# Optimization experiments

Hardware: AMD Instinct MI355X
Metric: run time of the kernel (lower is better)

## Reference

```python
import jax, jax.numpy as jnp
import numpy as np

SIGMA = 16.0


def setup_inputs() -> dict:
    key = jax.random.key(0)
    k1, k2, k3 = jax.random.split(key, 3)
    B, T, D = 8, 2048, 1024
    x = jax.random.normal(k1, (B, T, D), dtype=jnp.float32)
    posv = jax.random.randint(k2, (B, T), 0, 64, dtype=jnp.int32)
    posh = jax.random.randint(k3, (B, T), 0, 64, dtype=jnp.int32)
    return {"x": x, "posv": posv, "posh": posh}


def reference(x, posv, posh):
    # pos: [B, T, 2] float, as in torch.stack([posv, posh], -1).float()
    pos = jnp.stack([posv, posh], axis=-1).astype(jnp.float32)
    # pairwise squared distances: [B, T, T]
    diff = pos[:, :, None, :] - pos[:, None, :, :]
    dist_sq = jnp.sum(diff * diff, axis=-1)
    kernel = jnp.exp(-dist_sq / (2.0 * SIGMA * SIGMA))
    kernel = kernel / jnp.sum(kernel, axis=-1, keepdims=True)
    # dropout is identity in eval mode
    return jnp.einsum("bts,bsd->btd", kernel, x)
```

## Files before the change

kernel.cpp:

```cpp
#include <hip/hip_runtime.h>
#include <hip/hip_bf16.h>

#define NB 8
#define NT 2048
#define ND 1024
#define CAP 2048

typedef unsigned short ushort_t;
using short8 = __attribute__((ext_vector_type(8))) short;
using f32x4  = __attribute__((ext_vector_type(4))) float;

__device__ __forceinline__ ushort_t f2bf(float f) {
    __hip_bfloat16 h = __float2bfloat16(f);
    return *reinterpret_cast<ushort_t*>(&h);
}
__device__ __forceinline__ float bf2f(ushort_t u) {
    unsigned int v = ((unsigned int)u) << 16;
    return __int_as_float((int)v);
}


#define OFF_G2     256
#define OFF_AFH    768
#define OFF_AFL    8960
#define OFF_CNTV   17152
#define OFF_CNTH   19200
#define OFF_INVDEN 21248
#define OFF_GOFF   152320
#define OFF_TOKV   160512
#define OFF_TOKH   4354816
#define OFF_TOKV2  8549120
#define OFF_B1     12743424
#define B1_SLAB    ((size_t)64 * 64 * 1024 * 2)

__global__ __launch_bounds__(256) void k1_bucket(
    const int* __restrict__ posv, const int* __restrict__ posh,
    int* __restrict__ tokv, int* __restrict__ tokh,
    int* __restrict__ cntv, int* __restrict__ cnth,
    float* __restrict__ gbase, ushort_t* __restrict__ AfH,
    ushort_t* __restrict__ AfL)
{
    int b    = blockIdx.x >> 5;
    int blk  = blockIdx.x & 31;
    int wave = threadIdx.x >> 6;
    int lane = threadIdx.x & 63;

    if (blockIdx.x == 0) {
        if (threadIdx.x < 192) {
            int k = (int)threadIdx.x - 64;
            float v = 0.0f;
            if (k >= 0 && k < 127) {
                int r = k - 63;
                v = expf(-(float)(r * r) * (1.0f / 512.0f));
            }
            gbase[threadIdx.x] = v;
        }
#pragma unroll
        for (int p = 0; p < 16; p++) {
            int pos = (p << 8) + (int)threadIdx.x;
            int i   = pos & 7;
            int ln  = (pos >> 3) & 63;
            int ks  = (pos >> 9) & 1;
            int w   = pos >> 10;
            int q   = (w << 4) + (ln & 15);
            int k   = (ks << 5) + ((i >> 2) << 4) + ((ln >> 4) << 2) + (i & 3);
            int dlt = q - k;
            float g = expf(-(float)(dlt * dlt) * (1.0f / 512.0f));
            ushort_t hi = f2bf(g);
            AfH[pos] = hi;
            AfL[pos] = f2bf(g - bf2f(hi));
        }
    }

    int task   = blk * 4 + wave;
    int bucket = task & 63;
    int use_ph = task >> 6;
    const int* pos  = use_ph ? posh : posv;
    const int* opos = use_ph ? posv : posh;
    int* tok = (use_ph ? tokh : tokv) + ((size_t)(b * 64 + bucket)) * CAP;
    int* cnt = use_ph ? cnth : cntv;

    int vals[32];
#pragma unroll
    for (int k = 0; k < 32; k++) vals[k] = pos[b * NT + k * 64 + lane];

    unsigned long long lmask = (1ull << lane) - 1ull;
    int cursor = 0;
#pragma unroll 4
    for (int k = 0; k < 32; k++) {
        bool hit = (vals[k] == bucket);
        unsigned long long m = __ballot(hit);
        if (hit) {
            int t = k * 64 + lane;
            tok[cursor + __popcll(m & lmask)] = t | (opos[b * NT + t] << 16);
        }
        cursor += (int)__popcll(m);
    }
    if (lane == 0) cnt[b * 64 + bucket] = cursor;
}

__global__ __launch_bounds__(256) void k1b_group(
    const int* __restrict__ tokv, const int* __restrict__ cntv,
    int* __restrict__ tokv2, int4* __restrict__ goff)
{
    int bucket = blockIdx.x * 4 + (threadIdx.x >> 6);
    int lane   = threadIdx.x & 63;
    int n = cntv[bucket];
    const int* src = tokv + (size_t)bucket * CAP;
    int* dst = tokv2 + (size_t)bucket * CAP;
    unsigned long long lmask = (1ull << lane) - 1ull;

    int cnt0 = 0, cnt1 = 0, cnt2 = 0, cnt3 = 0;
    for (int base = 0; base < n; base += 64) {
        bool valid = base + lane < n;
        int pk = valid ? src[base + lane] : 0;
        int grp = (pk >> 20) & 3;
        cnt0 += (int)__popcll(__ballot(valid && grp == 0));
        cnt1 += (int)__popcll(__ballot(valid && grp == 1));
        cnt2 += (int)__popcll(__ballot(valid && grp == 2));
        cnt3 += (int)__popcll(__ballot(valid && grp == 3));
    }
    int s1 = cnt0, s2 = cnt0 + cnt1, s3 = cnt0 + cnt1 + cnt2;
    if (lane == 0) goff[bucket] = make_int4(0, s1, s2, s3);

    int c0 = 0, c1 = s1, c2 = s2, c3 = s3;
    for (int base = 0; base < n; base += 64) {
        bool valid = base + lane < n;
        int pk = valid ? src[base + lane] : 0;
        int grp = (pk >> 20) & 3;
        unsigned long long m0 = __ballot(valid && grp == 0);
        unsigned long long m1 = __ballot(valid && grp == 1);
        unsigned long long m2 = __ballot(valid && grp == 2);
        unsigned long long m3 = __ballot(valid && grp == 3);
        if (valid) {
            int p;
            if      (grp == 0) p = c0 + (int)__popcll(m0 & lmask);
            else if (grp == 1) p = c1 + (int)__popcll(m1 & lmask);
            else if (grp == 2) p = c2 + (int)__popcll(m2 & lmask);
            else               p = c3 + (int)__popcll(m3 & lmask);
            dst[p] = pk;
        }
        c0 += (int)__popcll(m0); c1 += (int)__popcll(m1);
        c2 += (int)__popcll(m2); c3 += (int)__popcll(m3);
    }
}

__global__ __launch_bounds__(256) void kden(
    const int* __restrict__ posv, const int* __restrict__ posh,
    const float* __restrict__ G2f, float* __restrict__ invden, int b0)
{
    int b   = b0 + (blockIdx.x >> 3);
    int phg = blockIdx.x & 7;
    int tid = threadIdx.x;

    __shared__ int   hist[64][64];
    __shared__ float g2s[128];
    __shared__ float tmp[64][8];

#pragma unroll
    for (int k = 0; k < 16; k++) ((int*)hist)[tid + (k << 8)] = 0;
    if (tid < 128) g2s[tid] = G2f[tid];
    __syncthreads();
#pragma unroll
    for (int k = 0; k < 8; k++) {
        int t = (k << 8) + tid;
        atomicAdd(&hist[posv[b * NT + t]][posh[b * NT + t]], 1);
    }
    __syncthreads();
#pragma unroll
    for (int c = 0; c < 2; c++) {
        int cell = (c << 8) + tid;
        int j    = cell >> 3;
        int phl  = cell & 7;
        int ph   = (phg << 3) + phl;
        float s = 0.f;
        for (int k = 0; k < 64; k++)
            s += (float)hist[j][k] * g2s[63 + k - ph];
        tmp[j][phl] = s;
    }
    __syncthreads();
#pragma unroll
    for (int c = 0; c < 2; c++) {
        int cell = (c << 8) + tid;
        int pv   = cell >> 3;
        int phl  = cell & 7;
        int ph   = (phg << 3) + phl;
        float s = 0.f;
        for (int j = 0; j < 64; j++)
            s += g2s[63 + j - pv] * tmp[j][phl];
        invden[(b * 64 + pv) * 64 + ph] = 1.0f / s;
    }
}

__device__ __forceinline__ short8 ldsBfrag(const ushort_t* rowp, int ks, int g4) {
    const ushort_t* p = rowp + (ks << 5) + g4;
    uint2 lo = *(const uint2*)(p);
    uint2 hi = *(const uint2*)(p + 16);
    uint4 pk; pk.x = lo.x; pk.y = lo.y; pk.z = hi.x; pk.w = hi.y;
    return __builtin_bit_cast(short8, pk);
}

__global__ __launch_bounds__(256) void k2_convh(
    const float* __restrict__ x,
    const int* __restrict__ tokv2, const int* __restrict__ cntv,
    const int4* __restrict__ goff,
    const ushort_t* __restrict__ AfH, const ushort_t* __restrict__ AfL,
    ushort_t* __restrict__ B1, int b0)
{
    int pv   = blockIdx.x & 63;
    int dc   = (blockIdx.x >> 6) & 15;
    int b    = b0 + (blockIdx.x >> 10);
    int tid  = threadIdx.x;
    int lane = tid & 63;
    int w    = tid >> 6;
    int d0   = dc << 6;

    __shared__ float    S[64][65];
    __shared__ ushort_t S16[64][68];

#pragma unroll
    for (int k = 0; k < 17; k++) {
        int idx = (k << 8) + tid;
        if (idx < 64 * 65) ((float*)S)[idx] = 0.f;
    }
    __syncthreads();

    int bucket = (b << 6) + pv;
    int n = cntv[bucket];
    const int* toks = tokv2 + (size_t)bucket * CAP;
    const float* xb = x + (((size_t)b * NT) << 10) + d0 + lane;

    int4 go = goff[bucket];
    int gs = (w == 0) ? go.x : (w == 1) ? go.y : (w == 2) ? go.z : go.w;
    int ge = (w == 3) ? n   : (w == 0) ? go.y : (w == 1) ? go.z : go.w;

    for (int win = gs; win < ge; win += 64) {
        int wn  = ge - win; if (wn > 64) wn = 64;
        int pkv = toks[win + lane];
        for (int i = 0; i < wn; i += 8) {
            int m = wn - i; if (m > 8) m = 8;
            int pk[8]; float xv[8];
#pragma unroll
            for (int j = 0; j < 8; j++)
                pk[j] = __builtin_amdgcn_readlane(pkv, i + j);
#pragma unroll
            for (int j = 0; j < 8; j++)
                if (j < m) xv[j] = xb[(size_t)(pk[j] & 0xffff) << 10];
#pragma unroll
            for (int j = 0; j < 8; j++)
                if (j < m) S[lane][pk[j] >> 16] += xv[j];
        }
    }
    __syncthreads();

    {
        int r  = tid & 63;
        int c0 = (tid >> 6) << 4;
#pragma unroll
        for (int c = 0; c < 16; c++)
            S16[r][c0 + c] = f2bf(S[r][c0 + c]);
    }
    __syncthreads();

    short8 ahi[2], alo[2];
#pragma unroll
    for (int ks = 0; ks < 2; ks++) {
        int idx = ((((w << 1) + ks) << 6) + lane) << 3;
        ahi[ks] = *(const short8*)(AfH + idx);
        alo[ks] = *(const short8*)(AfL + idx);
    }
    int g4 = (lane >> 4) << 2;
    int qbase = (w << 4) + g4;

    f32x4 accs[4];
#pragma unroll
    for (int nt = 0; nt < 4; nt++) {
        const ushort_t* rowp = &S16[(nt << 4) + (lane & 15)][0];
        f32x4 acc = {0.f, 0.f, 0.f, 0.f};
#pragma unroll
        for (int ks = 0; ks < 2; ks++) {
            short8 bf = ldsBfrag(rowp, ks, g4);
            acc = __builtin_amdgcn_mfma_f32_16x16x32_bf16(ahi[ks], bf, acc, 0, 0, 0);
            acc = __builtin_amdgcn_mfma_f32_16x16x32_bf16(alo[ks], bf, acc, 0, 0, 0);
        }
        accs[nt] = acc;
    }
    __syncthreads();

#pragma unroll
    for (int nt = 0; nt < 4; nt++)
#pragma unroll
        for (int reg = 0; reg < 4; reg++)
            S16[qbase + reg][(nt << 4) + (lane & 15)] = f2bf(accs[nt][reg]);
    __syncthreads();

    ushort_t* B1p = B1 + (((size_t)(b - b0)) << 22) + (((size_t)pv) << 10) + d0;
#pragma unroll
    for (int pass = 0; pass < 2; pass++) {
        int row = (pass << 5) + (tid >> 3);
        int col = (tid & 7) << 3;
        uint4 v = *(const uint4*)(&S16[row][col]);
        *reinterpret_cast<uint4*>(B1p + ((size_t)row << 16) + col) = v;
    }
}

__global__ __launch_bounds__(256) void k3_convv(
    const int* __restrict__ tokh, const int* __restrict__ cnth,
    const ushort_t* __restrict__ AfH, const ushort_t* __restrict__ AfL,
    const ushort_t* __restrict__ B1, const float* __restrict__ invden,
    float* __restrict__ out, int b0)
{
    int ph   = blockIdx.x & 63;
    int dc   = (blockIdx.x >> 6) & 15;
    int b    = b0 + (blockIdx.x >> 10);
    int tid  = threadIdx.x;
    int lane = tid & 63;
    int w    = tid >> 6;
    int d0   = dc << 6;

    int n = cnth[(b << 6) + ph];
    if (n == 0) return;

    __shared__ ushort_t u16[64][68];
    __shared__ float    y[64][65];

    const ushort_t* B1b = B1 + (((size_t)(b - b0)) << 22) + (((size_t)ph) << 16)
                        + d0 + lane;
#pragma unroll
    for (int it = 0; it < 16; it++) {
        int j = (w << 4) + it;
        u16[lane][j] = B1b[(size_t)j << 10];
    }
    __syncthreads();

    short8 ahi[2], alo[2];
#pragma unroll
    for (int ks = 0; ks < 2; ks++) {
        int idx = ((((w << 1) + ks) << 6) + lane) << 3;
        ahi[ks] = *(const short8*)(AfH + idx);
        alo[ks] = *(const short8*)(AfL + idx);
    }
    int g4 = (lane >> 4) << 2;
    int qbase = (w << 4) + g4;

#pragma unroll
    for (int nt = 0; nt < 4; nt++) {
        const ushort_t* rowp = &u16[(nt << 4) + (lane & 15)][0];
        f32x4 acc = {0.f, 0.f, 0.f, 0.f};
#pragma unroll
        for (int ks = 0; ks < 2; ks++) {
            short8 bf = ldsBfrag(rowp, ks, g4);
            acc = __builtin_amdgcn_mfma_f32_16x16x32_bf16(ahi[ks], bf, acc, 0, 0, 0);
            acc = __builtin_amdgcn_mfma_f32_16x16x32_bf16(alo[ks], bf, acc, 0, 0, 0);
        }
#pragma unroll
        for (int reg = 0; reg < 4; reg++)
            y[qbase + reg][(nt << 4) + (lane & 15)] = acc[reg];
    }
    __syncthreads();

    const int* toks = tokh + ((size_t)((b << 6) + ph)) * CAP;
    float* outb = out + (((size_t)b * NT) << 10) + d0 + lane;
    const float* ivb = invden + ((b << 6) << 6) + ph;

    int nch = (n + 3) >> 2;
    for (int c = w; c < nch; c += 4) {
        int i0 = c << 2;
        int4 M = *(const int4*)(toks + i0);
        int pk[4];
        pk[0] = __builtin_amdgcn_readfirstlane(M.x);
        pk[1] = __builtin_amdgcn_readfirstlane(M.y);
        pk[2] = __builtin_amdgcn_readfirstlane(M.z);
        pk[3] = __builtin_amdgcn_readfirstlane(M.w);
#pragma unroll
        for (int j = 0; j < 4; j++) {
            if (i0 + j < n) {
                int t   = pk[j] & 0xffff;
                int pvt = pk[j] >> 16;
                float iv = ivb[pvt << 6];
                outb[(size_t)t << 10] = y[pvt][lane] * iv;
            }
        }
    }
}

__global__ __launch_bounds__(256) void k_naive(
    const float* __restrict__ x, const int* __restrict__ posv,
    const int* __restrict__ posh, float* __restrict__ out)
{
    int t   = blockIdx.x & (NT - 1);
    int b   = blockIdx.x >> 11;
    int tid = threadIdx.x;

    __shared__ float s_w[NT];
    __shared__ float s_red[256];

    int pvt = posv[b * NT + t];
    int pht = posh[b * NT + t];

    float dsum = 0.0f;
    for (int s = tid; s < NT; s += 256) {
        int dv = pvt - posv[b * NT + s];
        int dh = pht - posh[b * NT + s];
        float w = expf(-(float)(dv * dv + dh * dh) * (1.0f / 512.0f));
        s_w[s] = w;
        dsum += w;
    }
    s_red[tid] = dsum;
    __syncthreads();
    for (int off = 128; off > 0; off >>= 1) {
        if (tid < off) s_red[tid] += s_red[tid + off];
        __syncthreads();
    }
    float inv = 1.0f / s_red[0];

    float a0 = 0.f, a1 = 0.f, a2 = 0.f, a3 = 0.f;
    for (int s = 0; s < NT; s++) {
        float w = s_w[s];
        const float* xr = x + (((size_t)(b * NT + s)) << 10);
        a0 = fmaf(w, xr[tid + 0],   a0);
        a1 = fmaf(w, xr[tid + 256], a1);
        a2 = fmaf(w, xr[tid + 512], a2);
        a3 = fmaf(w, xr[tid + 768], a3);
    }
    size_t ob = (((size_t)(b * NT + t)) << 10) + tid;
    out[ob + 0]   = a0 * inv;
    out[ob + 256] = a1 * inv;
    out[ob + 512] = a2 * inv;
    out[ob + 768] = a3 * inv;
}

extern "C" void kernel_launch(void* const* d_in, const int* in_sizes, int n_in,
                              void* d_out, int out_size, void* d_ws, size_t ws_size,
                              hipStream_t stream) {
    const float* x    = (const float*)d_in[0];
    const int*   posv = (const int*)d_in[1];
    const int*   posh = (const int*)d_in[2];
    float*       out  = (float*)d_out;

    char* ws = (char*)d_ws;
    float*    gbase  = (float*)ws;
    float*    G2f    = (float*)(ws + OFF_G2);
    ushort_t* AfH    = (ushort_t*)(ws + OFF_AFH);
    ushort_t* AfL    = (ushort_t*)(ws + OFF_AFL);
    int*      cntv   = (int*)(ws + OFF_CNTV);
    int*      cnth   = (int*)(ws + OFF_CNTH);
    float*    invden = (float*)(ws + OFF_INVDEN);
    int4*     goff   = (int4*)(ws + OFF_GOFF);
    int*      tokv   = (int*)(ws + OFF_TOKV);
    int*      tokh   = (int*)(ws + OFF_TOKH);
    int*      tokv2  = (int*)(ws + OFF_TOKV2);
    ushort_t* B1     = (ushort_t*)(ws + OFF_B1);

    const size_t needFull = (size_t)OFF_B1 + (size_t)NB * B1_SLAB;
    const size_t needLoop = (size_t)OFF_B1 + B1_SLAB;

    if (ws_size >= needFull) {
        k1_bucket<<<NB * 32, 256, 0, stream>>>(posv, posh, tokv, tokh, cntv, cnth,
                                               gbase, AfH, AfL);
        k1b_group<<<NB * 16, 256, 0, stream>>>(tokv, cntv, tokv2, goff);
        kden<<<NB * 8, 256, 0, stream>>>(posv, posh, G2f, invden, 0);
        k2_convh<<<NB * 1024, 256, 0, stream>>>(x, tokv2, cntv, goff, AfH, AfL, B1, 0);
        k3_convv<<<NB * 1024, 256, 0, stream>>>(tokh, cnth, AfH, AfL, B1, invden, out, 0);
    } else if (ws_size >= needLoop) {
        k1_bucket<<<NB * 32, 256, 0, stream>>>(posv, posh, tokv, tokh, cntv, cnth,
                                               gbase, AfH, AfL);
        k1b_group<<<NB * 16, 256, 0, stream>>>(tokv, cntv, tokv2, goff);
        for (int b = 0; b < NB; b++) {
            kden<<<8, 256, 0, stream>>>(posv, posh, G2f, invden, b);
            k2_convh<<<1024, 256, 0, stream>>>(x, tokv2, cntv, goff, AfH, AfL, B1, b);
            k3_convv<<<1024, 256, 0, stream>>>(tokh, cnth, AfH, AfL, B1, invden, out, b);
        }
    } else {
        k_naive<<<NB * NT, 256, 0, stream>>>(x, posv, posh, out);
    }
}
```

Before: 81.07 us.

## Alias LDS buffers in conv kernels and prefetch first gather before zeroing

In k2_convh and k3_convv, the float accumulation buffer and the bf16 staging buffer now share one LDS allocation. Values are moved through registers with an extra barrier so the two buffers do not overlap in time. This roughly halves shared memory per block, so more blocks can be resident per CU. k2 also issues the first window's token load and global x gathers before the LDS zeroing and its barrier, hiding that latency. The cost is extra barriers and more live registers (accs and vals), which could reduce occupancy in turn.

```diff
diff --git a/kernel.cpp b/kernel.cpp
--- a/kernel.cpp
+++ b/kernel.cpp
@@ -215,15 +215,9 @@
     int w    = tid >> 6;
     int d0   = dc << 6;
 
-    __shared__ float    S[64][65];
-    __shared__ ushort_t S16[64][68];
-
-#pragma unroll
-    for (int k = 0; k < 17; k++) {
-        int idx = (k << 8) + tid;
-        if (idx < 64 * 65) ((float*)S)[idx] = 0.f;
-    }
-    __syncthreads();
+    __shared__ float ldsf[64 * 65];
+    float    (*S)[65]   = (float(*)[65])ldsf;
+    ushort_t (*S16)[68] = (ushort_t(*)[68])ldsf;
 
     int bucket = (b << 6) + pv;
     int n = cntv[bucket];
@@ -234,15 +228,47 @@
     int gs = (w == 0) ? go.x : (w == 1) ? go.y : (w == 2) ? go.z : go.w;
     int ge = (w == 3) ? n   : (w == 0) ? go.y : (w == 1) ? go.z : go.w;
 
-    for (int win = gs; win < ge; win += 64) {
-        int wn  = ge - win; if (wn > 64) wn = 64;
-        int pkv = toks[win + lane];
+    int wn0 = ge - gs; if (wn0 < 0) wn0 = 0; if (wn0 > 64) wn0 = 64;
+    int m0  = wn0 > 8 ? 8 : wn0;
+    int pkv = (wn0 > 0) ? toks[gs + lane] : 0;
+    int pk0[8]; float xv0[8];
+#pragma unroll
+    for (int j = 0; j < 8; j++) pk0[j] = __builtin_amdgcn_readlane(pkv, j);
+#pragma unroll
+    for (int j = 0; j < 8; j++)
+        if (j < m0) xv0[j] = xb[(size_t)(pk0[j] & 0xffff) << 10];
+
+#pragma unroll
+    for (int k = 0; k < 17; k++) {
+        int idx = (k << 8) + tid;
+        if (idx < 64 * 65) ldsf[idx] = 0.f;
+    }
+    __syncthreads();
+
+#pragma unroll
+    for (int j = 0; j < 8; j++)
+        if (j < m0) S[lane][pk0[j] >> 16] += xv0[j];
+
+    for (int i = 8; i < wn0; i += 8) {
+        int m = wn0 - i; if (m > 8) m = 8;
+        int pk[8]; float xv[8];
+#pragma unroll
+        for (int j = 0; j < 8; j++) pk[j] = __builtin_amdgcn_readlane(pkv, i + j);
+#pragma unroll
+        for (int j = 0; j < 8; j++)
+            if (j < m) xv[j] = xb[(size_t)(pk[j] & 0xffff) << 10];
+#pragma unroll
+        for (int j = 0; j < 8; j++)
+            if (j < m) S[lane][pk[j] >> 16] += xv[j];
+    }
+    for (int win = gs + 64; win < ge; win += 64) {
+        int wn = ge - win; if (wn > 64) wn = 64;
+        int pkw = toks[win + lane];
         for (int i = 0; i < wn; i += 8) {
             int m = wn - i; if (m > 8) m = 8;
             int pk[8]; float xv[8];
 #pragma unroll
-            for (int j = 0; j < 8; j++)
-                pk[j] = __builtin_amdgcn_readlane(pkv, i + j);
+            for (int j = 0; j < 8; j++) pk[j] = __builtin_amdgcn_readlane(pkw, i + j);
 #pragma unroll
             for (int j = 0; j < 8; j++)
                 if (j < m) xv[j] = xb[(size_t)(pk[j] & 0xffff) << 10];
@@ -256,9 +282,12 @@
     {
         int r  = tid & 63;
         int c0 = (tid >> 6) << 4;
-#pragma unroll
-        for (int c = 0; c < 16; c++)
-            S16[r][c0 + c] = f2bf(S[r][c0 + c]);
+        float vals[16];
+#pragma unroll
+        for (int c = 0; c < 16; c++) vals[c] = S[r][c0 + c];
+        __syncthreads();
+#pragma unroll
+        for (int c = 0; c < 16; c++) S16[r][c0 + c] = f2bf(vals[c]);
     }
     __syncthreads();
 
@@ -321,8 +350,9 @@
     int n = cnth[(b << 6) + ph];
     if (n == 0) return;
 
-    __shared__ ushort_t u16[64][68];
-    __shared__ float    y[64][65];
+    __shared__ float ldsf[64 * 65];
+    ushort_t (*u16)[68] = (ushort_t(*)[68])ldsf;
+    float    (*y)[65]   = (float(*)[65])ldsf;
 
     const ushort_t* B1b = B1 + (((size_t)(b - b0)) << 22) + (((size_t)ph) << 16)
                         + d0 + lane;
@@ -343,6 +373,7 @@
     int g4 = (lane >> 4) << 2;
     int qbase = (w << 4) + g4;
 
+    f32x4 accs[4];
 #pragma unroll
     for (int nt = 0; nt < 4; nt++) {
         const ushort_t* rowp = &u16[(nt << 4) + (lane & 15)][0];
@@ -353,10 +384,15 @@
             acc = __builtin_amdgcn_mfma_f32_16x16x32_bf16(ahi[ks], bf, acc, 0, 0, 0);
             acc = __builtin_amdgcn_mfma_f32_16x16x32_bf16(alo[ks], bf, acc, 0, 0, 0);
         }
+        accs[nt] = acc;
+    }
+    __syncthreads();
+
+#pragma unroll
+    for (int nt = 0; nt < 4; nt++)
 #pragma unroll
         for (int reg = 0; reg < 4; reg++)
-            y[qbase + reg][(nt << 4) + (lane & 15)] = acc[reg];
-    }
+            y[qbase + reg][(nt << 4) + (lane & 15)] = accs[nt][reg];
     __syncthreads();
 
     const int* toks = tokh + ((size_t)((b << 6) + ph)) * CAP;
```

Measured after the change: 78.20 us. 3.5% less time.

## Fuse denominator into bucket kernel, accumulate conv in registers, shrink LDS

Applied to the files above, without the earlier changes.

The denominator kernel is folded into the bucketing launch as extra blocks. It now computes its Gaussian table inline instead of reading it from the workspace, which removes one launch and one dependency. In the horizontal conv, the shared-memory scatter-add array is replaced by per-wave register accumulators using a select-add across 16 slots, which cuts LDS footprint, the zeroing pass and a barrier. Occupancy is hinted at 4 via launch bounds. The vertical conv aliases its two LDS buffers to save shared memory, at the cost of an extra barrier and holding MFMA results in registers.

```diff
diff --git a/kernel.cpp b/kernel.cpp
--- a/kernel.cpp
+++ b/kernel.cpp
@@ -33,13 +33,68 @@
 #define OFF_B1     12743424
 #define B1_SLAB    ((size_t)64 * 64 * 1024 * 2)
 
+__device__ __forceinline__ void kden_body(
+    int kb, const int* __restrict__ posv, const int* __restrict__ posh,
+    float* __restrict__ invden, int b0)
+{
+    int b   = b0 + (kb >> 3);
+    int phg = kb & 7;
+    int tid = threadIdx.x;
+
+    __shared__ int   hist[64][64];
+    __shared__ float g2s[128];
+    __shared__ float tmp[64][8];
+
+#pragma unroll
+    for (int k = 0; k < 16; k++) ((int*)hist)[tid + (k << 8)] = 0;
+    if (tid < 128) {
+        int k = tid, r = k - 63;
+        g2s[tid] = (k < 127) ? expf(-(float)(r * r) * (1.0f / 512.0f)) : 0.0f;
+    }
+    __syncthreads();
+#pragma unroll
+    for (int k = 0; k < 8; k++) {
+        int t = (k << 8) + tid;
+        atomicAdd(&hist[posv[b * NT + t]][posh[b * NT + t]], 1);
+    }
+    __syncthreads();
+#pragma unroll
+    for (int c = 0; c < 2; c++) {
+        int cell = (c << 8) + tid;
+        int j    = cell >> 3;
+        int phl  = cell & 7;
+        int ph   = (phg << 3) + phl;
+        float s = 0.f;
+        for (int k = 0; k < 64; k++)
+            s += (float)hist[j][k] * g2s[63 + k - ph];
+        tmp[j][phl] = s;
+    }
+    __syncthreads();
+#pragma unroll
+    for (int c = 0; c < 2; c++) {
+        int cell = (c << 8) + tid;
+        int pv   = cell >> 3;
+        int phl  = cell & 7;
+        int ph   = (phg << 3) + phl;
+        float s = 0.f;
+        for (int j = 0; j < 64; j++)
+            s += g2s[63 + j - pv] * tmp[j][phl];
+        invden[(b * 64 + pv) * 64 + ph] = 1.0f / s;
+    }
+}
+
 __global__ __launch_bounds__(256) void k1_bucket(
     const int* __restrict__ posv, const int* __restrict__ posh,
     int* __restrict__ tokv, int* __restrict__ tokh,
     int* __restrict__ cntv, int* __restrict__ cnth,
     float* __restrict__ gbase, ushort_t* __restrict__ AfH,
-    ushort_t* __restrict__ AfL)
-{
+    ushort_t* __restrict__ AfL, float* __restrict__ invden, int nbkt)
+{
+    if ((int)blockIdx.x >= nbkt) {
+        kden_body((int)blockIdx.x - nbkt, posv, posh, invden, 0);
+        return;
+    }
+
     int b    = blockIdx.x >> 5;
     int blk  = blockIdx.x & 31;
     int wave = threadIdx.x >> 6;
@@ -97,6 +152,13 @@
         cursor += (int)__popcll(m);
     }
     if (lane == 0) cnt[b * 64 + bucket] = cursor;
+}
+
+__global__ __launch_bounds__(256) void kden(
+    const int* __restrict__ posv, const int* __restrict__ posh,
+    float* __restrict__ invden, int b0)
+{
+    kden_body((int)blockIdx.x, posv, posh, invden, b0);
 }
 
 __global__ __launch_bounds__(256) void k1b_group(
@@ -145,53 +207,6 @@
     }
 }
 
-__global__ __launch_bounds__(256) void kden(
-    const int* __restrict__ posv, const int* __restrict__ posh,
-    const float* __restrict__ G2f, float* __restrict__ invden, int b0)
-{
-    int b   = b0 + (blockIdx.x >> 3);
-    int phg = blockIdx.x & 7;
-    int tid = threadIdx.x;
-
-    __shared__ int   hist[64][64];
-    __shared__ float g2s[128];
-    __shared__ float tmp[64][8];
-
-#pragma unroll
-    for (int k = 0; k < 16; k++) ((int*)hist)[tid + (k << 8)] = 0;
-    if (tid < 128) g2s[tid] = G2f[tid];
-    __syncthreads();
-#pragma unroll
-    for (int k = 0; k < 8; k++) {
-        int t = (k << 8) + tid;
-        atomicAdd(&hist[posv[b * NT + t]][posh[b * NT + t]], 1);
-    }
-    __syncthreads();
-#pragma unroll
-    for (int c = 0; c < 2; c++) {
-        int cell = (c << 8) + tid;
-        int j    = cell >> 3;
-        int phl  = cell & 7;
-        int ph   = (phg << 3) + phl;
-        float s = 0.f;
-        for (int k = 0; k < 64; k++)
-            s += (float)hist[j][k] * g2s[63 + k - ph];
-        tmp[j][phl] = s;
-    }
-    __syncthreads();
-#pragma unroll
-    for (int c = 0; c < 2; c++) {
-        int cell = (c << 8) + tid;
-        int pv   = cell >> 3;
-        int phl  = cell & 7;
-        int ph   = (phg << 3) + phl;
-        float s = 0.f;
-        for (int j = 0; j < 64; j++)
-            s += g2s[63 + j - pv] * tmp[j][phl];
-        invden[(b * 64 + pv) * 64 + ph] = 1.0f / s;
-    }
-}
-
 __device__ __forceinline__ short8 ldsBfrag(const ushort_t* rowp, int ks, int g4) {
     const ushort_t* p = rowp + (ks << 5) + g4;
     uint2 lo = *(const uint2*)(p);
@@ -200,7 +215,7 @@
     return __builtin_bit_cast(short8, pk);
 }
 
-__global__ __launch_bounds__(256) void k2_convh(
+__global__ __launch_bounds__(256, 4) void k2_convh(
     const float* __restrict__ x,
     const int* __restrict__ tokv2, const int* __restrict__ cntv,
     const int4* __restrict__ goff,
@@ -215,15 +230,7 @@
     int w    = tid >> 6;
     int d0   = dc << 6;
 
-    __shared__ float    S[64][65];
     __shared__ ushort_t S16[64][68];
-
-#pragma unroll
-    for (int k = 0; k < 17; k++) {
-        int idx = (k << 8) + tid;
-        if (idx < 64 * 65) ((float*)S)[idx] = 0.f;
-    }
-    __syncthreads();
 
     int bucket = (b << 6) + pv;
     int n = cntv[bucket];
@@ -234,8 +241,20 @@
     int gs = (w == 0) ? go.x : (w == 1) ? go.y : (w == 2) ? go.z : go.w;
     int ge = (w == 3) ? n   : (w == 0) ? go.y : (w == 1) ? go.z : go.w;
 
+    short8 ahi[2], alo[2];
+#pragma unroll
+    for (int ks = 0; ks < 2; ks++) {
+        int idx = ((((w << 1) + ks) << 6) + lane) << 3;
+        ahi[ks] = *(const short8*)(AfH + idx);
+        alo[ks] = *(const short8*)(AfL + idx);
+    }
+
+    float acc[16];
+#pragma unroll
+    for (int q = 0; q < 16; q++) acc[q] = 0.f;
+
     for (int win = gs; win < ge; win += 64) {
-        int wn  = ge - win; if (wn > 64) wn = 64;
+        int wn = ge - win; if (wn > 64) wn = 64;
         int pkv = toks[win + lane];
         for (int i = 0; i < wn; i += 8) {
             int m = wn - i; if (m > 8) m = 8;
@@ -247,28 +266,25 @@
             for (int j = 0; j < 8; j++)
                 if (j < m) xv[j] = xb[(size_t)(pk[j] & 0xffff) << 10];
 #pragma unroll
-            for (int j = 0; j < 8; j++)
-                if (j < m) S[lane][pk[j] >> 16] += xv[j];
-        }
-    }
-    __syncthreads();
-
-    {
-        int r  = tid & 63;
-        int c0 = (tid >> 6) << 4;
-#pragma unroll
-        for (int c = 0; c < 16; c++)
-            S16[r][c0 + c] = f2bf(S[r][c0 + c]);
-    }
-    __syncthreads();
-
-    short8 ahi[2], alo[2];
-#pragma unroll
-    for (int ks = 0; ks < 2; ks++) {
-        int idx = ((((w << 1) + ks) << 6) + lane) << 3;
-        ahi[ks] = *(const short8*)(AfH + idx);
-        alo[ks] = *(const short8*)(AfL + idx);
-    }
+            for (int j = 0; j < 8; j++) {
+                if (j < m) {
+                    int phl = (pk[j] >> 16) & 15;
+#pragma unroll
+                    for (int q = 0; q < 16; q++)
+                        acc[q] += (q == phl) ? xv[j] : 0.0f;
+                }
+            }
+        }
+    }
+
+#pragma unroll
+    for (int h = 0; h < 8; h++) {
+        unsigned int pkd = (unsigned int)f2bf(acc[2 * h])
+                         | ((unsigned int)f2bf(acc[2 * h + 1]) << 16);
+        *reinterpret_cast<unsigned int*>(&S16[lane][(w << 4) + 2 * h]) = pkd;
+    }
+    __syncthreads();
+
     int g4 = (lane >> 4) << 2;
     int qbase = (w << 4) + g4;
 
@@ -276,14 +292,14 @@
 #pragma unroll
     for (int nt = 0; nt < 4; nt++) {
         const ushort_t* rowp = &S16[(nt << 4) + (lane & 15)][0];
-        f32x4 acc = {0.f, 0.f, 0.f, 0.f};
+        f32x4 a = {0.f, 0.f, 0.f, 0.f};
 #pragma unroll
         for (int ks = 0; ks < 2; ks++) {
             short8 bf = ldsBfrag(rowp, ks, g4);
-            acc = __builtin_amdgcn_mfma_f32_16x16x32_bf16(ahi[ks], bf, acc, 0, 0, 0);
-            acc = __builtin_amdgcn_mfma_f32_16x16x32_bf16(alo[ks], bf, acc, 0, 0, 0);
-        }
-        accs[nt] = acc;
+            a = __builtin_amdgcn_mfma_f32_16x16x32_bf16(ahi[ks], bf, a, 0, 0, 0);
+            a = __builtin_amdgcn_mfma_f32_16x16x32_bf16(alo[ks], bf, a, 0, 0, 0);
+        }
+        accs[nt] = a;
     }
     __syncthreads();
 
@@ -321,8 +337,9 @@
     int n = cnth[(b << 6) + ph];
     if (n == 0) return;
 
-    __shared__ ushort_t u16[64][68];
-    __shared__ float    y[64][65];
+    __shared__ float ldsf[64 * 65];
+    ushort_t (*u16)[68] = (ushort_t(*)[68])ldsf;
+    float    (*y)[65]   = (float(*)[65])ldsf;
 
     const ushort_t* B1b = B1 + (((size_t)(b - b0)) << 22) + (((size_t)ph) << 16)
                         + d0 + lane;
@@ -343,20 +360,26 @@
     int g4 = (lane >> 4) << 2;
     int qbase = (w << 4) + g4;
 
+    f32x4 accs[4];
 #pragma unroll
     for (int nt = 0; nt < 4; nt++) {
         const ushort_t* rowp = &u16[(nt << 4) + (lane & 15)][0];
-        f32x4 acc = {0.f, 0.f, 0.f, 0.f};
+        f32x4 a = {0.f, 0.f, 0.f, 0.f};
 #pragma unroll
         for (int ks = 0; ks < 2; ks++) {
             short8 bf = ldsBfrag(rowp, ks, g4);
-            acc = __builtin_amdgcn_mfma_f32_16x16x32_bf16(ahi[ks], bf, acc, 0, 0, 0);
-            acc = __builtin_amdgcn_mfma_f32_16x16x32_bf16(alo[ks], bf, acc, 0, 0, 0);
-        }
+            a = __builtin_amdgcn_mfma_f32_16x16x32_bf16(ahi[ks], bf, a, 0, 0, 0);
+            a = __builtin_amdgcn_mfma_f32_16x16x32_bf16(alo[ks], bf, a, 0, 0, 0);
+        }
+        accs[nt] = a;
+    }
+    __syncthreads();
+
+#pragma unroll
+    for (int nt = 0; nt < 4; nt++)
 #pragma unroll
         for (int reg = 0; reg < 4; reg++)
-            y[qbase + reg][(nt << 4) + (lane & 15)] = acc[reg];
-    }
+            y[qbase + reg][(nt << 4) + (lane & 15)] = accs[nt][reg];
     __syncthreads();
 
     const int* toks = tokh + ((size_t)((b << 6) + ph)) * CAP;
@@ -440,7 +463,6 @@
 
     char* ws = (char*)d_ws;
     float*    gbase  = (float*)ws;
-    float*    G2f    = (float*)(ws + OFF_G2);
     ushort_t* AfH    = (ushort_t*)(ws + OFF_AFH);
     ushort_t* AfL    = (ushort_t*)(ws + OFF_AFL);
     int*      cntv   = (int*)(ws + OFF_CNTV);
@@ -456,18 +478,17 @@
     const size_t needLoop = (size_t)OFF_B1 + B1_SLAB;
 
     if (ws_size >= needFull) {
-        k1_bucket<<<NB * 32, 256, 0, stream>>>(posv, posh, tokv, tokh, cntv, cnth,
-                                               gbase, AfH, AfL);
+        k1_bucket<<<NB * 32 + NB * 8, 256, 0, stream>>>(
+            posv, posh, tokv, tokh, cntv, cnth, gbase, AfH, AfL, invden, NB * 32);
         k1b_group<<<NB * 16, 256, 0, stream>>>(tokv, cntv, tokv2, goff);
-        kden<<<NB * 8, 256, 0, stream>>>(posv, posh, G2f, invden, 0);
         k2_convh<<<NB * 1024, 256, 0, stream>>>(x, tokv2, cntv, goff, AfH, AfL, B1, 0);
         k3_convv<<<NB * 1024, 256, 0, stream>>>(tokh, cnth, AfH, AfL, B1, invden, out, 0);
     } else if (ws_size >= needLoop) {
-        k1_bucket<<<NB * 32, 256, 0, stream>>>(posv, posh, tokv, tokh, cntv, cnth,
-                                               gbase, AfH, AfL);
+        k1_bucket<<<NB * 32, 256, 0, stream>>>(
+            posv, posh, tokv, tokh, cntv, cnth, gbase, AfH, AfL, invden, NB * 32 + 1);
         k1b_group<<<NB * 16, 256, 0, stream>>>(tokv, cntv, tokv2, goff);
         for (int b = 0; b < NB; b++) {
-            kden<<<8, 256, 0, stream>>>(posv, posh, G2f, invden, b);
+            kden<<<8, 256, 0, stream>>>(posv, posh, invden, b);
             k2_convh<<<1024, 256, 0, stream>>>(x, tokv2, cntv, goff, AfH, AfL, B1, b);
             k3_convv<<<1024, 256, 0, stream>>>(tokh, cnth, AfH, AfL, B1, invden, out, b);
         }
```

Result: faster. 75.88 us (-6.4%).
